# Optimization experiments

Hardware: AMD Instinct MI355X
Metric: run time of the kernel (lower is better)

## Reference

```python
import jax, jax.numpy as jnp
import numpy as np

N_HEADS = 16
D_MODEL = 1024
D_HEAD = 64
MAX_SEQ_LEN = 1024


def setup_inputs() -> dict:
    key = jax.random.key(0)
    ks = jax.random.split(key, 7)
    std = np.sqrt(2.0 / (D_MODEL + D_HEAD)).astype(np.float32)
    hd = N_HEADS * D_HEAD
    # Weights stored as (in, out) so projection is x @ W (torch Linear y = x W^T).
    Wq = jax.random.normal(ks[0], (D_MODEL, hd), jnp.float32) * std
    Wk = jax.random.normal(ks[1], (D_MODEL, hd), jnp.float32) * std
    Wv = jax.random.normal(ks[2], (D_MODEL, hd), jnp.float32) * std
    Wo = jax.random.normal(ks[3], (hd, D_MODEL), jnp.float32) * (1.0 / np.sqrt(hd))
    bo = jnp.zeros((D_MODEL,), jnp.float32)
    rel_pos_bias = jax.random.normal(ks[4], (N_HEADS, MAX_SEQ_LEN), jnp.float32) * 0.02
    x = jax.random.normal(ks[5], (4, 1024, D_MODEL), jnp.float32)
    return {"x": x, "Wq": Wq, "Wk": Wk, "Wv": Wv, "Wo": Wo, "bo": bo,
            "rel_pos_bias": rel_pos_bias}


def _pos_bias(rel_pos_bias, T):
    # bias[h, i, j] = rel_pos_bias[h, MAX_SEQ_LEN - 1 - (i - j)] for j <= i, else 0
    i = jnp.arange(T)[:, None]
    j = jnp.arange(T)[None, :]
    idx = jnp.clip(MAX_SEQ_LEN - 1 - (i - j), 0, MAX_SEQ_LEN - 1)
    bias = rel_pos_bias[:, idx]                      # [H, T, T]
    return jnp.where((j <= i)[None], bias, 0.0)


def reference(x, Wq, Wk, Wv, Wo, bo, rel_pos_bias):
    B, T, _ = x.shape
    H, dh = N_HEADS, D_HEAD
    q = (x @ Wq).reshape(B, T, H, dh).transpose(0, 2, 1, 3)  # [B,H,T,dh]
    k = (x @ Wk).reshape(B, T, H, dh).transpose(0, 2, 1, 3)
    v = (x @ Wv).reshape(B, T, H, dh).transpose(0, 2, 1, 3)
    logits = jnp.einsum('bhqd,bhkd->bhqk', q, k)
    i = jnp.arange(T)[:, None]
    j = jnp.arange(T)[None, :]
    causal = jnp.where(j > i, -jnp.inf, 0.0)                 # [T,T]
    logits = logits + causal[None, None] + _pos_bias(rel_pos_bias, T)[None]
    logits = logits / dh                                     # note: /d_head, not sqrt
    probs = jax.nn.softmax(logits, axis=-1)
    out = jnp.einsum('bhqk,bhkd->bhqd', probs, v)            # [B,H,T,dh]
    out = out.transpose(0, 2, 1, 3).reshape(B, T, H * dh)
    return out @ Wo + bo
```

## Files before the change

kernel.cpp:

```cpp
#include <hip/hip_runtime.h>
#include <math.h>

#define BATCH 4
#define SEQ   1024
#define DM    1024
#define NH    16
#define DH    64
#define BT    (BATCH*SEQ)

typedef _Float16 f16x8 __attribute__((ext_vector_type(8)));
typedef _Float16 f16x4 __attribute__((ext_vector_type(4)));
typedef float    f32x4 __attribute__((ext_vector_type(4)));

#define GLL16(ldsdst, gsrc) \
  __builtin_amdgcn_global_load_lds((const __attribute__((address_space(1))) void*)(gsrc), \
                                   (__attribute__((address_space(3))) void*)(ldsdst), 16, 0, 0)

__global__ __launch_bounds__(256) void cvt_x(const float* __restrict__ x,
                                             _Float16* __restrict__ xh, int nquads)
{
    int i = blockIdx.x * blockDim.x + threadIdx.x;
    for (; i < nquads; i += gridDim.x * blockDim.x) {
        float4 f = ((const float4*)x)[i];
        f16x4 h;
        h[0] = (_Float16)f.x; h[1] = (_Float16)f.y;
        h[2] = (_Float16)f.z; h[3] = (_Float16)f.w;
        ((f16x4*)xh)[i] = h;
    }
}

__global__ __launch_bounds__(256) void cvt_wT(
    const float* __restrict__ W0, const float* __restrict__ W1,
    const float* __restrict__ W2, const float* __restrict__ W3,
    _Float16* __restrict__ T0, _Float16* __restrict__ T1,
    _Float16* __restrict__ T2, _Float16* __restrict__ T3)
{
    __shared__ _Float16 tile[64][72];
    const int z = blockIdx.z;
    const float* W = (z == 0) ? W0 : (z == 1) ? W1 : (z == 2) ? W2 : W3;
    _Float16*    T = (z == 0) ? T0 : (z == 1) ? T1 : (z == 2) ? T2 : T3;
    const int n0 = blockIdx.x * 64;
    const int k0 = blockIdx.y * 64;
    const int tid = threadIdx.x;
#pragma unroll
    for (int p = 0; p < 4; ++p) {
        int r = (tid >> 4) + p * 16;
        int c = (tid & 15) * 4;
        float4 f = *(const float4*)&W[(size_t)(k0 + r) * DM + n0 + c];
        f16x4 h;
        h[0] = (_Float16)f.x; h[1] = (_Float16)f.y;
        h[2] = (_Float16)f.z; h[3] = (_Float16)f.w;
        *(f16x4*)&tile[r][c] = h;
    }
    __syncthreads();
#pragma unroll
    for (int p = 0; p < 2; ++p) {
        int nr = (tid >> 3) + p * 32;
        int kc = (tid & 7) * 8;
        f16x8 vv;
#pragma unroll
        for (int i = 0; i < 8; ++i) vv[i] = tile[kc + i][nr];
        *(f16x8*)&T[(size_t)(n0 + nr) * DM + k0 + kc] = vv;
    }
}

template<int MODE>
__global__ __launch_bounds__(256) void gemm_mfma(
    const _Float16* __restrict__ A,
    const _Float16* __restrict__ B0, const _Float16* __restrict__ B1,
    const _Float16* __restrict__ B2,
    void* __restrict__ o0, void* __restrict__ o1, void* __restrict__ o2,
    const float* __restrict__ bias)
{
    __shared__ _Float16 As[128 * 32];
    __shared__ _Float16 Bs[128 * 32];

    const int tid = threadIdx.x;
    const int w   = tid >> 6;
    const int ln  = tid & 63;
    const int l15 = ln & 15;
    const int lg  = ln >> 4;
    const int wr  = w >> 1;
    const int wc  = w & 1;
    const int which = MODE ? (blockIdx.x >> 3) : 0;
    const int nl  = (blockIdx.x & 7) * 128;
    const int m0  = blockIdx.y * 128;

    const _Float16* Bt = (which == 0) ? B0 : (which == 1 ? B1 : B2);

    const int srow = ln >> 2;
    const int scol = (ln & 3) * 8;
    const _Float16* ga = A  + (size_t)(m0 + w * 32 + srow) * DM + scol;
    const _Float16* gb = Bt + (size_t)(nl + w * 32 + srow) * DM + scol;
    _Float16* la0 = &As[(w * 32 +  0) * 32];
    _Float16* la1 = &As[(w * 32 + 16) * 32];
    _Float16* lb0 = &Bs[(w * 32 +  0) * 32];
    _Float16* lb1 = &Bs[(w * 32 + 16) * 32];

    f32x4 acc[4][4];
#pragma unroll
    for (int i = 0; i < 4; ++i)
#pragma unroll
        for (int j = 0; j < 4; ++j) acc[i][j] = (f32x4){0.f, 0.f, 0.f, 0.f};

    for (int k0 = 0; k0 < DM; k0 += 32) {
        GLL16(la0, ga + k0);
        GLL16(la1, ga + k0 + (size_t)16 * DM);
        GLL16(lb0, gb + k0);
        GLL16(lb1, gb + k0 + (size_t)16 * DM);
        __syncthreads();

        f16x8 af[4], bf[4];
#pragma unroll
        for (int i = 0; i < 4; ++i)
            af[i] = *(const f16x8*)&As[(wr * 64 + i * 16 + l15) * 32 + lg * 8];
#pragma unroll
        for (int j = 0; j < 4; ++j)
            bf[j] = *(const f16x8*)&Bs[(wc * 64 + j * 16 + l15) * 32 + lg * 8];
#pragma unroll
        for (int i = 0; i < 4; ++i)
#pragma unroll
            for (int j = 0; j < 4; ++j)
                acc[i][j] = __builtin_amdgcn_mfma_f32_16x16x32_f16(af[i], bf[j], acc[i][j], 0, 0, 0);
        __syncthreads();
    }

    if (MODE == 1) {
        _Float16* outp = (which == 0) ? (_Float16*)o0
                        : (which == 1) ? (_Float16*)o1 : (_Float16*)o2;
        const float scale = (which == 0) ? 0.015625f : 1.0f;
#pragma unroll
        for (int i = 0; i < 4; ++i)
#pragma unroll
            for (int j = 0; j < 4; ++j) {
                int n  = nl + wc * 64 + j * 16 + l15;
                int hh = n >> 6, d = n & 63;
#pragma unroll
                for (int r = 0; r < 4; ++r) {
                    int m  = m0 + wr * 64 + i * 16 + lg * 4 + r;
                    int b_ = m >> 10, t_ = m & 1023;
                    outp[(((size_t)(b_ * NH + hh)) * SEQ + t_) * DH + d] =
                        (_Float16)(acc[i][j][r] * scale);
                }
            }
    } else {
        float* outp = (float*)o0;
#pragma unroll
        for (int i = 0; i < 4; ++i)
#pragma unroll
            for (int j = 0; j < 4; ++j) {
                int n = nl + wc * 64 + j * 16 + l15;
                float bz = bias[n];
#pragma unroll
                for (int r = 0; r < 4; ++r) {
                    int m = m0 + wr * 64 + i * 16 + lg * 4 + r;
                    outp[(size_t)m * DM + n] = acc[i][j][r] + bz;
                }
            }
    }
}

__global__ __launch_bounds__(256) void vtranspose(const _Float16* __restrict__ V,
                                                  _Float16* __restrict__ Vt)
{
    __shared__ _Float16 tile[64][72];
    const int bh = blockIdx.y;
    const int t0 = blockIdx.x * 64;
    const int tid = threadIdx.x;
    const int r = tid >> 3;
    const int c = (tid & 7) * 8;
    const size_t base = (size_t)bh * (SEQ * DH);
#pragma unroll
    for (int p = 0; p < 2; ++p) {
        int row = r + p * 32;
        *(f16x8*)&tile[row][c] = *(const f16x8*)&V[base + (size_t)(t0 + row) * DH + c];
    }
    __syncthreads();
#pragma unroll
    for (int p = 0; p < 2; ++p) {
        int d = r + p * 32;
        f16x8 vv;
#pragma unroll
        for (int i = 0; i < 8; ++i) vv[i] = tile[c + i][d];
        *(f16x8*)&Vt[base + (size_t)d * SEQ + t0 + c] = vv;
    }
}

__global__ __launch_bounds__(512) void attn_mfma(
    const _Float16* __restrict__ Q,
    const _Float16* __restrict__ K,
    const _Float16* __restrict__ Vt,
    const float* __restrict__ rpb,
    _Float16* __restrict__ ao)
{
    const int pr  = blockIdx.x;
    const int bh  = blockIdx.y;
    const int b_  = bh >> 4;
    const int h_  = bh & 15;
    const int tid = threadIdx.x;
    const int w   = tid >> 6;
    const int ln  = tid & 63;
    const int l15 = ln & 15;
    const int lg  = ln >> 4;

    __shared__ _Float16 Pb[8][16][72];
    __shared__ float rpb_s[SEQ];

    *(float2*)&rpb_s[tid * 2] = *(const float2*)&rpb[h_ * SEQ + tid * 2];
    __syncthreads();

    const size_t qkb = (size_t)bh * (SEQ * DH);
    const int qt  = (w < 4) ? pr : (15 - pr);
    const int qr0 = qt * 64 + (w & 3) * 16;

    f16x8 qa0, qa1;
    {
        const _Float16* qp = Q + qkb + (size_t)(qr0 + l15) * DH + lg * 8;
        qa0 = *(const f16x8*)qp;
        qa1 = *(const f16x8*)(qp + 32);
    }
    f32x4 acc[4];
    float mrow[4], lrow[4];
#pragma unroll
    for (int t = 0; t < 4; ++t) {
        acc[t] = (f32x4){0.f, 0.f, 0.f, 0.f};
        mrow[t] = -INFINITY;
        lrow[t] = 0.f;
    }
    const int ibase = qr0 + lg * 4;

#pragma unroll 1
    for (int kt = 0; kt <= qt; ++kt) {
        const _Float16* kp = K + qkb + (size_t)(kt * 64 + l15) * DH + lg * 8;
        f32x4 s[4];
#pragma unroll
        for (int st = 0; st < 4; ++st) {
            f16x8 kb0 = *(const f16x8*)(kp + st * 16 * DH);
            f16x8 kb1 = *(const f16x8*)(kp + st * 16 * DH + 32);
            f32x4 z = (f32x4){0.f, 0.f, 0.f, 0.f};
            z = __builtin_amdgcn_mfma_f32_16x16x32_f16(qa0, kb0, z, 0, 0, 0);
            z = __builtin_amdgcn_mfma_f32_16x16x32_f16(qa1, kb1, z, 0, 0, 0);
            s[st] = z;
        }
        const int bidx = 1023 - ibase + l15 + kt * 64;
        float tm[4] = {-INFINITY, -INFINITY, -INFINITY, -INFINITY};
#pragma unroll
        for (int st = 0; st < 4; ++st)
#pragma unroll
            for (int r = 0; r < 4; ++r) {
                int idx = bidx + st * 16 - r;
                float bv = rpb_s[idx <= 1023 ? idx : 1023];
                float val = (idx <= 1023) ? fmaf(bv, 0.015625f, s[st][r]) : -INFINITY;
                s[st][r] = val;
                tm[r] = fmaxf(tm[r], val);
            }
#pragma unroll
        for (int r = 0; r < 4; ++r) {
            tm[r] = fmaxf(tm[r], __shfl_xor(tm[r], 1, 16));
            tm[r] = fmaxf(tm[r], __shfl_xor(tm[r], 2, 16));
            tm[r] = fmaxf(tm[r], __shfl_xor(tm[r], 4, 16));
            tm[r] = fmaxf(tm[r], __shfl_xor(tm[r], 8, 16));
        }
        float corr[4], psum[4];
#pragma unroll
        for (int r = 0; r < 4; ++r) {
            float mn = fmaxf(mrow[r], tm[r]);
            corr[r]  = __expf(mrow[r] - mn);
            mrow[r]  = mn;
            psum[r]  = 0.f;
        }
#pragma unroll
        for (int st = 0; st < 4; ++st)
#pragma unroll
            for (int r = 0; r < 4; ++r) {
                float p = __expf(s[st][r] - mrow[r]);
                s[st][r] = p;
                psum[r] += p;
            }
#pragma unroll
        for (int r = 0; r < 4; ++r) {
            psum[r] += __shfl_xor(psum[r], 1, 16);
            psum[r] += __shfl_xor(psum[r], 2, 16);
            psum[r] += __shfl_xor(psum[r], 4, 16);
            psum[r] += __shfl_xor(psum[r], 8, 16);
            lrow[r] = lrow[r] * corr[r] + psum[r];
        }
#pragma unroll
        for (int t = 0; t < 4; ++t) {
            acc[t][0] *= corr[0]; acc[t][1] *= corr[1];
            acc[t][2] *= corr[2]; acc[t][3] *= corr[3];
        }
#pragma unroll
        for (int st = 0; st < 4; ++st)
#pragma unroll
            for (int r = 0; r < 4; ++r)
                Pb[w][lg * 4 + r][st * 16 + l15] = (_Float16)s[st][r];
        f16x8 pa0 = *(const f16x8*)&Pb[w][l15][lg * 8];
        f16x8 pa1 = *(const f16x8*)&Pb[w][l15][32 + lg * 8];
        const _Float16* vp = Vt + qkb + (size_t)l15 * SEQ + kt * 64 + lg * 8;
#pragma unroll
        for (int dt = 0; dt < 4; ++dt) {
            f16x8 vb0 = *(const f16x8*)(vp + dt * 16 * SEQ);
            f16x8 vb1 = *(const f16x8*)(vp + dt * 16 * SEQ + 32);
            acc[dt] = __builtin_amdgcn_mfma_f32_16x16x32_f16(pa0, vb0, acc[dt], 0, 0, 0);
            acc[dt] = __builtin_amdgcn_mfma_f32_16x16x32_f16(pa1, vb1, acc[dt], 0, 0, 0);
        }
    }
    _Float16* aop = ao + ((size_t)b_ * SEQ + ibase) * DM + h_ * DH + l15;
#pragma unroll
    for (int r = 0; r < 4; ++r) {
        float inv = 1.f / lrow[r];
#pragma unroll
        for (int dt = 0; dt < 4; ++dt)
            aop[(size_t)r * DM + dt * 16] = (_Float16)(acc[dt][r] * inv);
    }
}

extern "C" void kernel_launch(void* const* d_in, const int* in_sizes, int n_in,
                              void* d_out, int out_size, void* d_ws, size_t ws_size,
                              hipStream_t stream)
{
    (void)in_sizes; (void)n_in; (void)out_size; (void)ws_size;
    const float* x   = (const float*)d_in[0];
    const float* Wq  = (const float*)d_in[1];
    const float* Wk  = (const float*)d_in[2];
    const float* Wv  = (const float*)d_in[3];
    const float* Wo  = (const float*)d_in[4];
    const float* bo  = (const float*)d_in[5];
    const float* rpb = (const float*)d_in[6];
    float* out = (float*)d_out;

    char* ws = (char*)d_ws;
    _Float16* xh  = (_Float16*)(ws);
    _Float16* q   = (_Float16*)(ws + (8u  << 20));
    _Float16* k   = (_Float16*)(ws + (16u << 20));
    _Float16* v   = (_Float16*)(ws + (24u << 20));
    _Float16* vt  = (_Float16*)(ws + (32u << 20));
    _Float16* aoh = (_Float16*)(ws + (40u << 20));
    _Float16* wqt = (_Float16*)(ws + (48u << 20));
    _Float16* wkt = (_Float16*)(ws + (50u << 20));
    _Float16* wvt = (_Float16*)(ws + (52u << 20));
    _Float16* wot = (_Float16*)(ws + (54u << 20));

    cvt_x<<<2048, 256, 0, stream>>>(x, xh, BT * DM / 4);
    cvt_wT<<<dim3(16, 16, 4), 256, 0, stream>>>(Wq, Wk, Wv, Wo, wqt, wkt, wvt, wot);
    gemm_mfma<1><<<dim3(24, 32), 256, 0, stream>>>(xh, wqt, wkt, wvt, q, k, v, nullptr);
    vtranspose<<<dim3(SEQ / 64, BATCH * NH), 256, 0, stream>>>(v, vt);
    attn_mfma<<<dim3(8, BATCH * NH), 512, 0, stream>>>(q, k, vt, rpb, aoh);
    gemm_mfma<0><<<dim3(8, 32), 256, 0, stream>>>(aoh, wot, nullptr, nullptr, out, nullptr, nullptr, bo);
}
```

Before: 220.1 us.

## Split attention KV loop across wave pairs with split-K softmax merge

Each block now handles a single 64-row query tile. Pairs of waves split that tile's key tiles between even and odd indices, and at the end the partial softmax states (max, sum, accumulators) are merged through shared memory. This replaces pairing two query tiles per block for load balance. The grid doubles to 16x64 blocks, which raises parallelism and shortens each wave's serial KV chain. The cost is an extra barrier, a merge step, and an fp16 round-trip of the partial accumulators.

```diff
diff --git a/kernel.cpp b/kernel.cpp
--- a/kernel.cpp
+++ b/kernel.cpp
@@ -193,25 +193,27 @@
     const float* __restrict__ rpb,
     _Float16* __restrict__ ao)
 {
-    const int pr  = blockIdx.x;
+    const int qt  = 15 - blockIdx.x;
     const int bh  = blockIdx.y;
     const int b_  = bh >> 4;
     const int h_  = bh & 15;
     const int tid = threadIdx.x;
     const int w   = tid >> 6;
+    const int job = w >> 1;
+    const int s   = w & 1;
     const int ln  = tid & 63;
     const int l15 = ln & 15;
     const int lg  = ln >> 4;
 
     __shared__ _Float16 Pb[8][16][72];
+    __shared__ float mls[4][64][8];
     __shared__ float rpb_s[SEQ];
 
     *(float2*)&rpb_s[tid * 2] = *(const float2*)&rpb[h_ * SEQ + tid * 2];
     __syncthreads();
 
     const size_t qkb = (size_t)bh * (SEQ * DH);
-    const int qt  = (w < 4) ? pr : (15 - pr);
-    const int qr0 = qt * 64 + (w & 3) * 16;
+    const int qr0 = qt * 64 + job * 16;
 
     f16x8 qa0, qa1;
     {
@@ -230,9 +232,9 @@
     const int ibase = qr0 + lg * 4;
 
 #pragma unroll 1
-    for (int kt = 0; kt <= qt; ++kt) {
+    for (int kt = s; kt <= qt; kt += 2) {
         const _Float16* kp = K + qkb + (size_t)(kt * 64 + l15) * DH + lg * 8;
-        f32x4 s[4];
+        f32x4 sv[4];
 #pragma unroll
         for (int st = 0; st < 4; ++st) {
             f16x8 kb0 = *(const f16x8*)(kp + st * 16 * DH);
@@ -240,7 +242,7 @@
             f32x4 z = (f32x4){0.f, 0.f, 0.f, 0.f};
             z = __builtin_amdgcn_mfma_f32_16x16x32_f16(qa0, kb0, z, 0, 0, 0);
             z = __builtin_amdgcn_mfma_f32_16x16x32_f16(qa1, kb1, z, 0, 0, 0);
-            s[st] = z;
+            sv[st] = z;
         }
         const int bidx = 1023 - ibase + l15 + kt * 64;
         float tm[4] = {-INFINITY, -INFINITY, -INFINITY, -INFINITY};
@@ -250,8 +252,8 @@
             for (int r = 0; r < 4; ++r) {
                 int idx = bidx + st * 16 - r;
                 float bv = rpb_s[idx <= 1023 ? idx : 1023];
-                float val = (idx <= 1023) ? fmaf(bv, 0.015625f, s[st][r]) : -INFINITY;
-                s[st][r] = val;
+                float val = (idx <= 1023) ? fmaf(bv, 0.015625f, sv[st][r]) : -INFINITY;
+                sv[st][r] = val;
                 tm[r] = fmaxf(tm[r], val);
             }
 #pragma unroll
@@ -273,8 +275,8 @@
         for (int st = 0; st < 4; ++st)
 #pragma unroll
             for (int r = 0; r < 4; ++r) {
-                float p = __expf(s[st][r] - mrow[r]);
-                s[st][r] = p;
+                float p = __expf(sv[st][r] - mrow[r]);
+                sv[st][r] = p;
                 psum[r] += p;
             }
 #pragma unroll
@@ -294,7 +296,7 @@
         for (int st = 0; st < 4; ++st)
 #pragma unroll
             for (int r = 0; r < 4; ++r)
-                Pb[w][lg * 4 + r][st * 16 + l15] = (_Float16)s[st][r];
+                Pb[w][lg * 4 + r][st * 16 + l15] = (_Float16)sv[st][r];
         f16x8 pa0 = *(const f16x8*)&Pb[w][l15][lg * 8];
         f16x8 pa1 = *(const f16x8*)&Pb[w][l15][32 + lg * 8];
         const _Float16* vp = Vt + qkb + (size_t)l15 * SEQ + kt * 64 + lg * 8;
@@ -306,13 +308,43 @@
             acc[dt] = __builtin_amdgcn_mfma_f32_16x16x32_f16(pa1, vb1, acc[dt], 0, 0, 0);
         }
     }
-    _Float16* aop = ao + ((size_t)b_ * SEQ + ibase) * DM + h_ * DH + l15;
-#pragma unroll
-    for (int r = 0; r < 4; ++r) {
-        float inv = 1.f / lrow[r];
+
+    if (s == 1) {
+        _Float16* mb = &Pb[w][0][0];
 #pragma unroll
         for (int dt = 0; dt < 4; ++dt)
-            aop[(size_t)r * DM + dt * 16] = (_Float16)(acc[dt][r] * inv);
+#pragma unroll
+            for (int r = 0; r < 4; ++r)
+                mb[ln * 16 + dt * 4 + r] = (_Float16)acc[dt][r];
+#pragma unroll
+        for (int r = 0; r < 4; ++r) {
+            mls[job][ln][r]     = mrow[r];
+            mls[job][ln][4 + r] = lrow[r];
+        }
+    }
+    __syncthreads();
+    if (s == 0) {
+        const _Float16* mb = &Pb[w + 1][0][0];
+        float c0[4], c1[4];
+#pragma unroll
+        for (int r = 0; r < 4; ++r) {
+            float m1 = mls[job][ln][r];
+            float l1 = mls[job][ln][4 + r];
+            float mm = fmaxf(mrow[r], m1);
+            c0[r] = __expf(mrow[r] - mm);
+            c1[r] = __expf(m1 - mm);
+            lrow[r] = lrow[r] * c0[r] + l1 * c1[r];
+        }
+        _Float16* aop = ao + ((size_t)b_ * SEQ + ibase) * DM + h_ * DH + l15;
+#pragma unroll
+        for (int r = 0; r < 4; ++r) {
+            float inv = 1.f / lrow[r];
+#pragma unroll
+            for (int dt = 0; dt < 4; ++dt) {
+                float v = acc[dt][r] * c0[r] + (float)mb[ln * 16 + dt * 4 + r] * c1[r];
+                aop[(size_t)r * DM + dt * 16] = (_Float16)(v * inv);
+            }
+        }
     }
 }
 
@@ -346,6 +378,6 @@
     cvt_wT<<<dim3(16, 16, 4), 256, 0, stream>>>(Wq, Wk, Wv, Wo, wqt, wkt, wvt, wot);
     gemm_mfma<1><<<dim3(24, 32), 256, 0, stream>>>(xh, wqt, wkt, wvt, q, k, v, nullptr);
     vtranspose<<<dim3(SEQ / 64, BATCH * NH), 256, 0, stream>>>(v, vt);
-    attn_mfma<<<dim3(8, BATCH * NH), 512, 0, stream>>>(q, k, vt, rpb, aoh);
+    attn_mfma<<<dim3(16, BATCH * NH), 512, 0, stream>>>(q, k, vt, rpb, aoh);
     gemm_mfma<0><<<dim3(8, 32), 256, 0, stream>>>(aoh, wot, nullptr, nullptr, out, nullptr, nullptr, bo);
 }
```

Measured after the change: 267.6 us. +21.6%, slower.

## Transpose attention MFMA so each lane owns one query row

Applied to the files above, without the earlier changes.

Swaps the MFMA operand order so the score and output tiles are transposed and each lane holds values for a single query row. Row max and sum reductions then take two cross-lane shuffles instead of sixteen, and P is written to LDS and the output to global memory as packed 4-element vectors. The relative-position bias is prescaled by 1/64 into LDS and padded with large negative values, which removes the per-element clamp and causal select. The risk is correctness of the new index mapping, and masked entries use -1e30 instead of -inf.

```diff
diff --git a/kernel.cpp b/kernel.cpp
--- a/kernel.cpp
+++ b/kernel.cpp
@@ -204,115 +204,105 @@
     const int lg  = ln >> 4;
 
     __shared__ _Float16 Pb[8][16][72];
-    __shared__ float rpb_s[SEQ];
-
-    *(float2*)&rpb_s[tid * 2] = *(const float2*)&rpb[h_ * SEQ + tid * 2];
+    __shared__ float rpb2[1152];
+
+    {
+        float2 t = *(const float2*)&rpb[h_ * SEQ + tid * 2];
+        t.x *= 0.015625f; t.y *= 0.015625f;
+        *(float2*)&rpb2[tid * 2] = t;
+        if (tid < 128) rpb2[1024 + tid] = -1e30f;
+    }
     __syncthreads();
 
     const size_t qkb = (size_t)bh * (SEQ * DH);
     const int qt  = (w < 4) ? pr : (15 - pr);
     const int qr0 = qt * 64 + (w & 3) * 16;
+    const int i_  = qr0 + l15;
 
     f16x8 qa0, qa1;
     {
-        const _Float16* qp = Q + qkb + (size_t)(qr0 + l15) * DH + lg * 8;
+        const _Float16* qp = Q + qkb + (size_t)i_ * DH + lg * 8;
         qa0 = *(const f16x8*)qp;
         qa1 = *(const f16x8*)(qp + 32);
     }
-    f32x4 acc[4];
-    float mrow[4], lrow[4];
-#pragma unroll
-    for (int t = 0; t < 4; ++t) {
-        acc[t] = (f32x4){0.f, 0.f, 0.f, 0.f};
-        mrow[t] = -INFINITY;
-        lrow[t] = 0.f;
-    }
-    const int ibase = qr0 + lg * 4;
+    f32x4 accT[4];
+#pragma unroll
+    for (int dt = 0; dt < 4; ++dt) accT[dt] = (f32x4){0.f, 0.f, 0.f, 0.f};
+    float m = -INFINITY, l = 0.f;
 
 #pragma unroll 1
     for (int kt = 0; kt <= qt; ++kt) {
         const _Float16* kp = K + qkb + (size_t)(kt * 64 + l15) * DH + lg * 8;
-        f32x4 s[4];
+        f32x4 sv[4];
 #pragma unroll
         for (int st = 0; st < 4; ++st) {
             f16x8 kb0 = *(const f16x8*)(kp + st * 16 * DH);
             f16x8 kb1 = *(const f16x8*)(kp + st * 16 * DH + 32);
             f32x4 z = (f32x4){0.f, 0.f, 0.f, 0.f};
-            z = __builtin_amdgcn_mfma_f32_16x16x32_f16(qa0, kb0, z, 0, 0, 0);
-            z = __builtin_amdgcn_mfma_f32_16x16x32_f16(qa1, kb1, z, 0, 0, 0);
-            s[st] = z;
+            z = __builtin_amdgcn_mfma_f32_16x16x32_f16(kb0, qa0, z, 0, 0, 0);
+            z = __builtin_amdgcn_mfma_f32_16x16x32_f16(kb1, qa1, z, 0, 0, 0);
+            sv[st] = z;
         }
-        const int bidx = 1023 - ibase + l15 + kt * 64;
-        float tm[4] = {-INFINITY, -INFINITY, -INFINITY, -INFINITY};
+        const int bidx = 1023 - i_ + kt * 64 + lg * 4;
+        float tmax = -INFINITY;
 #pragma unroll
         for (int st = 0; st < 4; ++st)
 #pragma unroll
             for (int r = 0; r < 4; ++r) {
-                int idx = bidx + st * 16 - r;
-                float bv = rpb_s[idx <= 1023 ? idx : 1023];
-                float val = (idx <= 1023) ? fmaf(bv, 0.015625f, s[st][r]) : -INFINITY;
-                s[st][r] = val;
-                tm[r] = fmaxf(tm[r], val);
+                float v = sv[st][r] + rpb2[bidx + st * 16 + r];
+                sv[st][r] = v;
+                tmax = fmaxf(tmax, v);
             }
-#pragma unroll
-        for (int r = 0; r < 4; ++r) {
-            tm[r] = fmaxf(tm[r], __shfl_xor(tm[r], 1, 16));
-            tm[r] = fmaxf(tm[r], __shfl_xor(tm[r], 2, 16));
-            tm[r] = fmaxf(tm[r], __shfl_xor(tm[r], 4, 16));
-            tm[r] = fmaxf(tm[r], __shfl_xor(tm[r], 8, 16));
+        tmax = fmaxf(tmax, __shfl_xor(tmax, 16));
+        tmax = fmaxf(tmax, __shfl_xor(tmax, 32));
+        float mn   = fmaxf(m, tmax);
+        float corr = __expf(m - mn);
+        m = mn;
+        float ps = 0.f;
+#pragma unroll
+        for (int st = 0; st < 4; ++st)
+#pragma unroll
+            for (int r = 0; r < 4; ++r) {
+                float p = __expf(sv[st][r] - mn);
+                sv[st][r] = p;
+                ps += p;
+            }
+        ps += __shfl_xor(ps, 16);
+        ps += __shfl_xor(ps, 32);
+        l = l * corr + ps;
+#pragma unroll
+        for (int dt = 0; dt < 4; ++dt) {
+            accT[dt][0] *= corr; accT[dt][1] *= corr;
+            accT[dt][2] *= corr; accT[dt][3] *= corr;
         }
-        float corr[4], psum[4];
-#pragma unroll
-        for (int r = 0; r < 4; ++r) {
-            float mn = fmaxf(mrow[r], tm[r]);
-            corr[r]  = __expf(mrow[r] - mn);
-            mrow[r]  = mn;
-            psum[r]  = 0.f;
+#pragma unroll
+        for (int st = 0; st < 4; ++st) {
+            f16x4 pk;
+            pk[0] = (_Float16)sv[st][0]; pk[1] = (_Float16)sv[st][1];
+            pk[2] = (_Float16)sv[st][2]; pk[3] = (_Float16)sv[st][3];
+            *(f16x4*)&Pb[w][l15][st * 16 + lg * 4] = pk;
         }
-#pragma unroll
-        for (int st = 0; st < 4; ++st)
-#pragma unroll
-            for (int r = 0; r < 4; ++r) {
-                float p = __expf(s[st][r] - mrow[r]);
-                s[st][r] = p;
-                psum[r] += p;
-            }
-#pragma unroll
-        for (int r = 0; r < 4; ++r) {
-            psum[r] += __shfl_xor(psum[r], 1, 16);
-            psum[r] += __shfl_xor(psum[r], 2, 16);
-            psum[r] += __shfl_xor(psum[r], 4, 16);
-            psum[r] += __shfl_xor(psum[r], 8, 16);
-            lrow[r] = lrow[r] * corr[r] + psum[r];
-        }
-#pragma unroll
-        for (int t = 0; t < 4; ++t) {
-            acc[t][0] *= corr[0]; acc[t][1] *= corr[1];
-            acc[t][2] *= corr[2]; acc[t][3] *= corr[3];
-        }
-#pragma unroll
-        for (int st = 0; st < 4; ++st)
-#pragma unroll
-            for (int r = 0; r < 4; ++r)
-                Pb[w][lg * 4 + r][st * 16 + l15] = (_Float16)s[st][r];
-        f16x8 pa0 = *(const f16x8*)&Pb[w][l15][lg * 8];
-        f16x8 pa1 = *(const f16x8*)&Pb[w][l15][32 + lg * 8];
+        f16x8 pf0 = *(const f16x8*)&Pb[w][l15][lg * 8];
+        f16x8 pf1 = *(const f16x8*)&Pb[w][l15][32 + lg * 8];
         const _Float16* vp = Vt + qkb + (size_t)l15 * SEQ + kt * 64 + lg * 8;
 #pragma unroll
         for (int dt = 0; dt < 4; ++dt) {
             f16x8 vb0 = *(const f16x8*)(vp + dt * 16 * SEQ);
             f16x8 vb1 = *(const f16x8*)(vp + dt * 16 * SEQ + 32);
-            acc[dt] = __builtin_amdgcn_mfma_f32_16x16x32_f16(pa0, vb0, acc[dt], 0, 0, 0);
-            acc[dt] = __builtin_amdgcn_mfma_f32_16x16x32_f16(pa1, vb1, acc[dt], 0, 0, 0);
+            accT[dt] = __builtin_amdgcn_mfma_f32_16x16x32_f16(vb0, pf0, accT[dt], 0, 0, 0);
+            accT[dt] = __builtin_amdgcn_mfma_f32_16x16x32_f16(vb1, pf1, accT[dt], 0, 0, 0);
         }
     }
-    _Float16* aop = ao + ((size_t)b_ * SEQ + ibase) * DM + h_ * DH + l15;
-#pragma unroll
-    for (int r = 0; r < 4; ++r) {
-        float inv = 1.f / lrow[r];
-#pragma unroll
-        for (int dt = 0; dt < 4; ++dt)
-            aop[(size_t)r * DM + dt * 16] = (_Float16)(acc[dt][r] * inv);
+    float inv = 1.f / l;
+    _Float16* aop = ao + ((size_t)(b_ * SEQ + i_)) * DM + h_ * DH + lg * 4;
+#pragma unroll
+    for (int dt = 0; dt < 4; ++dt) {
+        f16x4 o4;
+        o4[0] = (_Float16)(accT[dt][0] * inv);
+        o4[1] = (_Float16)(accT[dt][1] * inv);
+        o4[2] = (_Float16)(accT[dt][2] * inv);
+        o4[3] = (_Float16)(accT[dt][3] * inv);
+        *(f16x4*)&aop[dt * 16] = o4;
     }
 }
 
```

Measured after the change: 216.1 us. About the same (-1.8%).
